# Performance work log

Hardware: AMD Instinct MI355X
Metric: run time of the kernel (lower is better)

Reference implementation:

```python
import jax, jax.numpy as jnp
import numpy as np
from jax.nn import relu, softplus, sigmoid

B, T, C, L = 256, 128, 16, 64
ENC, H, OBS_IN, NLAGS = 32, 64, 8, 24
SUBSTEPS = 2


def setup_inputs() -> dict:
    key = jax.random.key(0)
    ks = jax.random.split(key, 32)
    rn = lambda k, shp, s=0.1: jax.random.normal(k, shp, dtype=jnp.float32) * s
    return {
        "timestamps": jnp.linspace(0.0, 1.0, T, dtype=jnp.float32),
        "obs": rn(ks[0], (B, NLAGS, OBS_IN), 1.0),
        "coef_d": rn(ks[1], (B, T - 1, C)),
        "coef_c": rn(ks[2], (B, T - 1, C)),
        "coef_b": rn(ks[3], (B, T - 1, C)),
        "coef_a": rn(ks[4], (B, T - 1, C)),
        "gru_wih": rn(ks[5], (3 * H, OBS_IN)),
        "gru_whh": rn(ks[6], (3 * H, H)),
        "gru_bih": rn(ks[7], (3 * H,)),
        "gru_bhh": rn(ks[8], (3 * H,)),
        "gru_lin_w": rn(ks[9], (ENC, H)),
        "ie_w0": rn(ks[10], (128, ENC + C)),
        "ie_b0": rn(ks[11], (128,)),
        "ie_wh": rn(ks[12], (1, 128, 128)),
        "ie_bh": rn(ks[13], (1, 128)),
        "ie_wout": rn(ks[14], (L, 128)),
        "ie_bout": rn(ks[15], (L,)),
        "vf_w0": rn(ks[16], (128, L)),
        "vf_b0": rn(ks[17], (128,)),
        "vf_wh": rn(ks[18], (1, 128, 128)),
        "vf_bh": rn(ks[19], (1, 128)),
        "vf_wout": rn(ks[20], (L * C, 128)),
        "vf_bout": rn(ks[21], (L * C,)),
        "dec_w0": rn(ks[22], (L // 2, L)),
        "dec_b0": rn(ks[23], (L // 2,)),
        "dec_wh": rn(ks[24], (1, L // 2, L // 2)),
        "dec_bh": rn(ks[25], (1, L // 2)),
        "dec_wout": rn(ks[26], (8, L // 2)),
        "dec_bout": rn(ks[27], (8,)),
    }


def _mlp(x, w0, b0, wh, bh, wout, bout, act, fact):
    h = act(w0 @ x + b0)
    for i in range(wh.shape[0]):  # fixed small depth
        h = act(wh[i] @ h + bh[i])
    return fact(wout @ h + bout)


_ident = lambda v: v


def reference(timestamps, obs, coef_d, coef_c, coef_b, coef_a,
              gru_wih, gru_whh, gru_bih, gru_bhh, gru_lin_w,
              ie_w0, ie_b0, ie_wh, ie_bh, ie_wout, ie_bout,
              vf_w0, vf_b0, vf_wh, vf_bh, vf_wout, vf_bout,
              dec_w0, dec_b0, dec_wh, dec_bh, dec_wout, dec_bout):

    def single(obs_s, d_s, c_s, b_s, a_s):
        # --- GRU observation encoder ---
        def cell(h, x):
            gi = gru_wih @ x + gru_bih
            gh = gru_whh @ h + gru_bhh
            ir, iz, inn = jnp.split(gi, 3)
            hr, hz, hn = jnp.split(gh, 3)
            r = sigmoid(ir + hr)
            z = sigmoid(iz + hz)
            n = jnp.tanh(inn + r * hn)
            return (1.0 - z) * n + z * h, None
        hT, _ = jax.lax.scan(cell, jnp.zeros((H,), jnp.float32), obs_s)
        enc = gru_lin_w @ hT
        # control.evaluate(t0): cubic poly at frac=0 -> constant coeff a[0]
        x0 = a_s[0]
        y0 = _mlp(jnp.concatenate([enc, x0]), ie_w0, ie_b0, ie_wh, ie_bh, ie_wout, ie_bout, relu, _ident)

        def vf(y):
            return _mlp(y, vf_w0, vf_b0, vf_wh, vf_bh, vf_wout, vf_bout, softplus, jnp.tanh).reshape(L, C)

        js = jnp.arange(SUBSTEPS, dtype=jnp.float32)

        def interval(y, xs):
            t0, t1, di, ci, bi = xs
            hstep = (t1 - t0) / SUBSTEPS
            def f(frac, yy):
                dx = bi + 2.0 * ci * frac + 3.0 * di * frac * frac  # dX/dt on this interval
                return vf(yy) @ dx  # (L,)
            def sub(yy, j):  # one fixed Dopri5 step
                f0 = j * hstep
                k1 = f(f0, yy)
                k2 = f(f0 + hstep / 5, yy + hstep * (k1 / 5))
                k3 = f(f0 + 3 * hstep / 10, yy + hstep * (3 / 40 * k1 + 9 / 40 * k2))
                k4 = f(f0 + 4 * hstep / 5, yy + hstep * (44 / 45 * k1 - 56 / 15 * k2 + 32 / 9 * k3))
                k5 = f(f0 + 8 * hstep / 9, yy + hstep * (19372 / 6561 * k1 - 25360 / 2187 * k2 + 64448 / 6561 * k3 - 212 / 729 * k4))
                k6 = f(f0 + hstep, yy + hstep * (9017 / 3168 * k1 - 355 / 33 * k2 + 46732 / 5247 * k3 + 49 / 176 * k4 - 5103 / 18656 * k5))
                yn = yy + hstep * (35 / 384 * k1 + 500 / 1113 * k3 + 125 / 192 * k4 - 2187 / 6784 * k5 + 11 / 84 * k6)
                return yn, None
            y, _ = jax.lax.scan(jax.checkpoint(sub), y, js)
            return y, y

        xs = (timestamps[:-1], timestamps[1:], d_s, c_s, b_s)
        _, ys_rest = jax.lax.scan(interval, y0, xs)
        ys = jnp.concatenate([y0[None], ys_rest], axis=0)  # (T, L)
        dec = lambda yy: _mlp(yy, dec_w0, dec_b0, dec_wh, dec_bh, dec_wout, dec_bout, relu, _ident)
        return jax.vmap(dec)(ys)  # (T, state_size)

    return jax.vmap(single)(obs, coef_d, coef_c, coef_b, coef_a)  # (B, T, state_size)
```

## Files before the change

kernel.cpp:

```cpp
#include <hip/hip_runtime.h>
#include <hip/hip_fp16.h>

#define TPB 512

typedef _Float16 f16x8 __attribute__((ext_vector_type(8)));
typedef float f32x4 __attribute__((ext_vector_type(4)));

__device__ __forceinline__ float softplus_f(float x) {
    return fmaxf(x, 0.f) + __logf(1.f + __expf(-fabsf(x)));
}
__device__ __forceinline__ float tanh_f(float x) {
    float e = __expf(2.f * x);
    return 1.f - 2.f / (e + 1.f);
}
__device__ __forceinline__ float sigmoid_f(float x) {
    return 1.f / (1.f + __expf(-x));
}

__device__ __forceinline__ f32x4 mfma16(f16x8 a, f16x8 b, f32x4 c) {
    return __builtin_amdgcn_mfma_f32_16x16x32_f16(a, b, c, 0, 0, 0);
}

template <int CTRL>
__device__ __forceinline__ float dpp_add(float x) {
    int m = __builtin_amdgcn_update_dpp(0, __builtin_bit_cast(int, x), CTRL, 0xF, 0xF, true);
    return x + __builtin_bit_cast(float, m);
}

__global__ __launch_bounds__(TPB, 1) void ncde_kernel(
    const float* __restrict__ timestamps, const float* __restrict__ obs,
    const float* __restrict__ coef_d, const float* __restrict__ coef_c,
    const float* __restrict__ coef_b, const float* __restrict__ coef_a,
    const float* __restrict__ gru_wih, const float* __restrict__ gru_whh,
    const float* __restrict__ gru_bih, const float* __restrict__ gru_bhh,
    const float* __restrict__ gru_lin_w,
    const float* __restrict__ ie_w0, const float* __restrict__ ie_b0,
    const float* __restrict__ ie_wh, const float* __restrict__ ie_bh,
    const float* __restrict__ ie_wout, const float* __restrict__ ie_bout,
    const float* __restrict__ vf_w0, const float* __restrict__ vf_b0,
    const float* __restrict__ vf_wh, const float* __restrict__ vf_bh,
    const float* __restrict__ vf_wout, const float* __restrict__ vf_bout,
    const float* __restrict__ dec_w0, const float* __restrict__ dec_b0,
    const float* __restrict__ dec_wh, const float* __restrict__ dec_bh,
    const float* __restrict__ dec_wout, const float* __restrict__ dec_bout,
    float* __restrict__ out)
{
    const int b = blockIdx.x;
    const int tid = threadIdx.x;
    const int lane = tid & 63, wv = tid >> 6;
    const int m16 = lane & 15, g4 = lane >> 4;

    __shared__ __align__(16) float s_ysall[128][64];
    __shared__ __align__(16) float s_whh[192 * 65];
    __shared__ __align__(16) float s_wih[192 * 9];
    __shared__ __align__(16) float s_obs[24 * 8];
    __shared__ float s_gi[192];
    __shared__ float s_gh[192];
    __shared__ __align__(16) float s_y[64];
    __shared__ __align__(16) __half s_ysbh[64];
    __shared__ __align__(16) __half s_h1h[128];
    __shared__ __align__(16) __half s_h2h[128];
    __shared__ __align__(16) float s_V[1024];
    __shared__ __align__(16) float s_k[6][64];
    __shared__ float s_bi[16], s_ci[16], s_di[16];
    __shared__ __align__(16) float s_v48[48];
    __shared__ float s_m1[128], s_m2[128];

    for (int idx = tid; idx < 192 * 64; idx += TPB)
        s_whh[(idx >> 6) * 65 + (idx & 63)] = gru_whh[idx];
    for (int idx = tid; idx < 192 * 8; idx += TPB)
        s_wih[(idx >> 3) * 9 + (idx & 7)] = gru_wih[idx];
    if (tid < 24 * 8) s_obs[tid] = obs[(size_t)b * 192 + tid];
    const float bih_r = (tid < 192) ? gru_bih[tid] : 0.f;
    const float bhh_r = (tid < 192) ? gru_bhh[tid] : 0.f;
    if (tid < 64) s_y[tid] = 0.f;
    __syncthreads();

    for (int step = 0; step < 24; ++step) {
        if (tid < 192) {
            float gi = bih_r;
            const float* wr = &s_wih[tid * 9];
            const float* xr = &s_obs[step * 8];
#pragma unroll
            for (int j = 0; j < 8; ++j) gi = fmaf(wr[j], xr[j], gi);
            float g0 = bhh_r, g1 = 0.f, g2 = 0.f, g3 = 0.f;
            const float* hr = &s_whh[tid * 65];
#pragma unroll 4
            for (int j = 0; j < 64; j += 4) {
                g0 = fmaf(hr[j + 0], s_y[j + 0], g0);
                g1 = fmaf(hr[j + 1], s_y[j + 1], g1);
                g2 = fmaf(hr[j + 2], s_y[j + 2], g2);
                g3 = fmaf(hr[j + 3], s_y[j + 3], g3);
            }
            s_gi[tid] = gi;
            s_gh[tid] = (g0 + g1) + (g2 + g3);
        }
        __syncthreads();
        if (tid < 64) {
            float rg = sigmoid_f(s_gi[tid] + s_gh[tid]);
            float zg = sigmoid_f(s_gi[64 + tid] + s_gh[64 + tid]);
            float ng = tanh_f(s_gi[128 + tid] + rg * s_gh[128 + tid]);
            s_y[tid] = (1.f - zg) * ng + zg * s_y[tid];
        }
        __syncthreads();
    }

    if (tid < 32) {
        float e = 0.f;
        const float* wr = gru_lin_w + tid * 64;
        for (int j = 0; j < 64; ++j) e = fmaf(wr[j], s_y[j], e);
        s_v48[tid] = e;
    } else if (tid < 48) {
        s_v48[tid] = coef_a[(size_t)b * 127 * 16 + (tid - 32)];
    }
    __syncthreads();

    if (tid < 128) {
        float a = ie_b0[tid];
        const float* wr = ie_w0 + tid * 48;
        for (int j = 0; j < 48; ++j) a = fmaf(wr[j], s_v48[j], a);
        s_m1[tid] = fmaxf(a, 0.f);
    }
    __syncthreads();
    if (tid < 128) {
        float a = ie_bh[tid];
        const float* wr = ie_wh + tid * 128;
        for (int j = 0; j < 128; ++j) a = fmaf(wr[j], s_m1[j], a);
        s_m2[tid] = fmaxf(a, 0.f);
    }
    __syncthreads();
    if (tid < 64) {
        float a = ie_bout[tid];
        const float* wr = ie_wout + tid * 128;
        for (int j = 0; j < 128; ++j) a = fmaf(wr[j], s_m2[j], a);
        s_y[tid] = a;
        s_ysbh[tid] = __float2half_rn(a);
        s_ysall[0][tid] = a;
    }
    __syncthreads();

    f16x8 aw0[2], awh[4], awq[8][4];
    {
        const int row = wv * 16 + m16;
#pragma unroll
        for (int f = 0; f < 2; ++f) {
            f16x8 a;
#pragma unroll
            for (int j = 0; j < 8; ++j)
                a[j] = (_Float16)vf_w0[row * 64 + f * 32 + g4 * 8 + j];
            aw0[f] = a;
        }
#pragma unroll
        for (int f = 0; f < 4; ++f) {
            f16x8 a;
#pragma unroll
            for (int j = 0; j < 8; ++j)
                a[j] = (_Float16)vf_wh[row * 128 + f * 32 + g4 * 8 + j];
            awh[f] = a;
        }
#pragma unroll
        for (int i = 0; i < 8; ++i) {
            const int rq = (wv * 8 + i) * 16 + m16;
#pragma unroll
            for (int f = 0; f < 4; ++f) {
                f16x8 a;
#pragma unroll
                for (int j = 0; j < 8; ++j)
                    a[j] = (_Float16)vf_wout[(size_t)rq * 128 + f * 32 + g4 * 8 + j];
                awq[i][f] = a;
            }
        }
    }
    const float4 bw0 = *(const float4*)(vf_b0 + wv * 16 + g4 * 4);
    const float4 bwh = *(const float4*)(vf_bh + wv * 16 + g4 * 4);
    const float bo0 = vf_bout[2 * tid], bo1 = vf_bout[2 * tid + 1];
    const int l_idx = tid >> 3;
    const int c0 = 2 * (tid & 7);

    const size_t cofs = (size_t)b * 127 * 16;

#define KS(m) s_k[m][tid]
#define YS_PHASE(...)                                                          \
    do {                                                                       \
        if (tid < 64) {                                                        \
            float yv = s_y[tid];                                               \
            __VA_ARGS__;                                                       \
            s_ysbh[tid] = __float2half_rn(yv);                                 \
        }                                                                      \
        __syncthreads();                                                       \
    } while (0)

#define MFMA_STAGE(S, CC)                                                      \
    do {                                                                       \
        {                          \
            f16x8 b0 = *(const f16x8*)((const char*)s_ysbh + g4 * 16);         \
            f16x8 b1 = *(const f16x8*)((const char*)s_ysbh + 64 + g4 * 16);    \
            f32x4 acc = {0.f, 0.f, 0.f, 0.f};                                  \
            acc = mfma16(aw0[0], b0, acc);                                     \
            acc = mfma16(aw0[1], b1, acc);                                     \
            if (m16 == 0) {                                                    \
                __half q0 = __float2half_rn(softplus_f(acc[0] + bw0.x));       \
                __half q1 = __float2half_rn(softplus_f(acc[1] + bw0.y));       \
                __half q2 = __float2half_rn(softplus_f(acc[2] + bw0.z));       \
                __half q3 = __float2half_rn(softplus_f(acc[3] + bw0.w));       \
                uint2 pk;                                                      \
                pk.x = (unsigned)__half_as_ushort(q0) | ((unsigned)__half_as_ushort(q1) << 16); \
                pk.y = (unsigned)__half_as_ushort(q2) | ((unsigned)__half_as_ushort(q3) << 16); \
                *(uint2*)(&s_h1h[wv * 16 + g4 * 4]) = pk;                      \
            }                                                                  \
        }                                                                      \
        __syncthreads();                                                       \
        {                                                    \
            f32x4 acc = {0.f, 0.f, 0.f, 0.f};                                  \
            _Pragma("unroll")                                                  \
            for (int f = 0; f < 4; ++f) {                                      \
                f16x8 bf = *(const f16x8*)((const char*)s_h1h + f * 64 + g4 * 16); \
                acc = mfma16(awh[f], bf, acc);                                 \
            }                                                                  \
            if (m16 == 0) {                                                    \
                __half q0 = __float2half_rn(softplus_f(acc[0] + bwh.x));       \
                __half q1 = __float2half_rn(softplus_f(acc[1] + bwh.y));       \
                __half q2 = __float2half_rn(softplus_f(acc[2] + bwh.z));       \
                __half q3 = __float2half_rn(softplus_f(acc[3] + bwh.w));       \
                uint2 pk;                                                      \
                pk.x = (unsigned)__half_as_ushort(q0) | ((unsigned)__half_as_ushort(q1) << 16); \
                pk.y = (unsigned)__half_as_ushort(q2) | ((unsigned)__half_as_ushort(q3) << 16); \
                *(uint2*)(&s_h2h[wv * 16 + g4 * 4]) = pk;                      \
            }                                                                  \
        }                                                                      \
        __syncthreads();                                                       \
        {                     \
            f16x8 bf[4];                                                       \
            _Pragma("unroll")                                                  \
            for (int f = 0; f < 4; ++f)                                        \
                bf[f] = *(const f16x8*)((const char*)s_h2h + f * 64 + g4 * 16); \
            _Pragma("unroll")                                                  \
            for (int i = 0; i < 8; ++i) {                                      \
                f32x4 acc = {0.f, 0.f, 0.f, 0.f};                              \
                acc = mfma16(awq[i][0], bf[0], acc);                           \
                acc = mfma16(awq[i][1], bf[1], acc);                           \
                acc = mfma16(awq[i][2], bf[2], acc);                           \
                acc = mfma16(awq[i][3], bf[3], acc);                           \
                if (m16 == 0)                                                  \
                    *(f32x4*)(&s_V[(wv * 8 + i) * 16 + g4 * 4]) = acc;         \
            }                                                                  \
        }                                                                      \
        __syncthreads();                                                       \
        {              \
            float2 vp = *(const float2*)(&s_V[l_idx * 16 + c0]);               \
            float v0 = tanh_f(vp.x + bo0);                                     \
            float v1 = tanh_f(vp.y + bo1);                                     \
            float frac = fmaf((CC), hstep, f0);                                \
            float dx0 = fmaf(3.f * s_di[c0], frac * frac,                      \
                             fmaf(2.f * s_ci[c0], frac, s_bi[c0]));            \
            float dx1 = fmaf(3.f * s_di[c0 + 1], frac * frac,                  \
                             fmaf(2.f * s_ci[c0 + 1], frac, s_bi[c0 + 1]));    \
            float p = fmaf(v0, dx0, v1 * dx1);                                 \
            p = dpp_add<0xB1>(p);                                              \
            p = dpp_add<0x4E>(p);                                              \
            p = dpp_add<0x141>(p);                                             \
            if ((tid & 7) == 0) s_k[S][l_idx] = p;                             \
        }                                                                      \
        __syncthreads();                                                       \
    } while (0)

#pragma unroll 1
    for (int t = 0; t < 127; ++t) {
        if (tid < 16) s_bi[tid] = coef_b[cofs + t * 16 + tid];
        else if (tid < 32) s_ci[tid - 16] = coef_c[cofs + t * 16 + (tid - 16)];
        else if (tid < 48) s_di[tid - 32] = coef_d[cofs + t * 16 + (tid - 32)];
        const float t0 = timestamps[t], t1 = timestamps[t + 1];
        const float hstep = (t1 - t0) * 0.5f;

#pragma unroll 1
        for (int sub = 0; sub < 2; ++sub) {
            const float f0 = (float)sub * hstep;

            MFMA_STAGE(0, 0.f);
            YS_PHASE(yv = fmaf(hstep * 0.2f, KS(0), yv));
            MFMA_STAGE(1, 0.2f);
            YS_PHASE(yv = fmaf(hstep, fmaf(3.f / 40.f, KS(0), (9.f / 40.f) * KS(1)), yv));
            MFMA_STAGE(2, 0.3f);
            YS_PHASE(yv = fmaf(hstep, fmaf(44.f / 45.f, KS(0),
                          fmaf(-56.f / 15.f, KS(1), (32.f / 9.f) * KS(2))), yv));
            MFMA_STAGE(3, 0.8f);
            YS_PHASE(yv = fmaf(hstep, fmaf(19372.f / 6561.f, KS(0),
                          fmaf(-25360.f / 2187.f, KS(1),
                          fmaf(64448.f / 6561.f, KS(2), (-212.f / 729.f) * KS(3)))), yv));
            MFMA_STAGE(4, 8.f / 9.f);
            YS_PHASE(yv = fmaf(hstep, fmaf(9017.f / 3168.f, KS(0),
                          fmaf(-355.f / 33.f, KS(1),
                          fmaf(46732.f / 5247.f, KS(2),
                          fmaf(49.f / 176.f, KS(3), (-5103.f / 18656.f) * KS(4))))), yv));
            MFMA_STAGE(5, 1.f);

            if (tid < 64) {
                float yv = s_y[tid];
                yv = fmaf(hstep * (35.f / 384.f), s_k[0][tid], yv);
                yv = fmaf(hstep * (500.f / 1113.f), s_k[2][tid], yv);
                yv = fmaf(hstep * (125.f / 192.f), s_k[3][tid], yv);
                yv = fmaf(hstep * (-2187.f / 6784.f), s_k[4][tid], yv);
                yv = fmaf(hstep * (11.f / 84.f), s_k[5][tid], yv);
                s_y[tid] = yv;
                s_ysbh[tid] = __float2half_rn(yv);
                if (sub == 1) s_ysall[t + 1][tid] = yv;
            }
            __syncthreads();
        }
    }

    const int wid = tid >> 6, lane2 = tid & 63;
    for (int t = wid; t < 128; t += 8) {
        const float* yy = s_ysall[t];
        float h1d = 0.f;
        if (lane2 < 32) {
            float a = dec_b0[lane2];
            const float* wr = dec_w0 + lane2 * 64;
            for (int j = 0; j < 64; ++j) a = fmaf(wr[j], yy[j], a);
            h1d = fmaxf(a, 0.f);
        }
        float a2 = (lane2 < 32) ? dec_bh[lane2] : 0.f;
#pragma unroll 8
        for (int j = 0; j < 32; ++j) {
            float hj = __shfl(h1d, j);
            if (lane2 < 32) a2 = fmaf(dec_wh[lane2 * 32 + j], hj, a2);
        }
        float h2d = fmaxf(a2, 0.f);
        float o = (lane2 < 8) ? dec_bout[lane2] : 0.f;
#pragma unroll 8
        for (int j = 0; j < 32; ++j) {
            float hj = __shfl(h2d, j);
            if (lane2 < 8) o = fmaf(dec_wout[lane2 * 32 + j], hj, o);
        }
        if (lane2 < 8) out[(size_t)b * 1024 + t * 8 + lane2] = o;
    }
}

extern "C" void kernel_launch(void* const* d_in, const int* in_sizes, int n_in,
                              void* d_out, int out_size, void* d_ws, size_t ws_size,
                              hipStream_t stream) {
    const float* p[29];
    for (int i = 0; i < 29; ++i) p[i] = (const float*)d_in[i];
    ncde_kernel<<<256, TPB, 0, stream>>>(
        p[0], p[1], p[2], p[3], p[4], p[5], p[6], p[7], p[8], p[9], p[10],
        p[11], p[12], p[13], p[14], p[15], p[16], p[17], p[18], p[19], p[20],
        p[21], p[22], p[23], p[24], p[25], p[26], p[27], p[28],
        (float*)d_out);
}
```

Before: 2.855 ms.

## Replace output-layer MFMA with per-thread fp16 dot2 and fuse stage updates

The 1024x128 vector-field output layer is now computed per thread: each thread holds its two weight rows packed as fp16 pairs in registers and uses fdot2 against the hidden vector in shared memory. This removes the s_V staging buffer and one barrier per stage. The RK stage-state update is folded into the lane that writes each k value, which removes the separate YS phase and its barrier. The cost is 128 extra VGPRs of weights per thread, which raises register pressure and may spill, plus more scalar ALU work in place of matrix instructions.

```diff
diff --git a/kernel.cpp b/kernel.cpp
--- a/kernel.cpp
+++ b/kernel.cpp
@@ -3,8 +3,25 @@
 
 #define TPB 512
 
+typedef _Float16 h2v __attribute__((ext_vector_type(2)));
 typedef _Float16 f16x8 __attribute__((ext_vector_type(8)));
 typedef float f32x4 __attribute__((ext_vector_type(4)));
+
+__device__ __forceinline__ float dot2f(unsigned int a, unsigned int b, float c) {
+#if __has_builtin(__builtin_amdgcn_fdot2)
+    return __builtin_amdgcn_fdot2(__builtin_bit_cast(h2v, a), __builtin_bit_cast(h2v, b), c, false);
+#else
+    float2 af = __half22float2(__builtin_bit_cast(__half2, a));
+    float2 bf = __half22float2(__builtin_bit_cast(__half2, b));
+    return fmaf(af.y, bf.y, fmaf(af.x, bf.x, c));
+#endif
+}
+
+__device__ __forceinline__ unsigned int pack2(float a, float b) {
+    unsigned int lo = (unsigned int)__half_as_ushort(__float2half_rn(a));
+    unsigned int hi = (unsigned int)__half_as_ushort(__float2half_rn(b));
+    return lo | (hi << 16);
+}
 
 __device__ __forceinline__ float softplus_f(float x) {
     return fmaxf(x, 0.f) + __logf(1.f + __expf(-fabsf(x)));
@@ -60,7 +77,6 @@
     __shared__ __align__(16) __half s_ysbh[64];
     __shared__ __align__(16) __half s_h1h[128];
     __shared__ __align__(16) __half s_h2h[128];
-    __shared__ __align__(16) float s_V[1024];
     __shared__ __align__(16) float s_k[6][64];
     __shared__ float s_bi[16], s_ci[16], s_di[16];
     __shared__ __align__(16) float s_v48[48];
@@ -139,7 +155,16 @@
     }
     __syncthreads();
 
-    f16x8 aw0[2], awh[4], awq[8][4];
+    unsigned int wq0[64], wq1[64];
+    {
+        const float* r0 = vf_wout + (size_t)(2 * tid) * 128;
+#pragma unroll
+        for (int j = 0; j < 64; ++j) wq0[j] = pack2(r0[2 * j], r0[2 * j + 1]);
+        const float* r1 = r0 + 128;
+#pragma unroll
+        for (int j = 0; j < 64; ++j) wq1[j] = pack2(r1[2 * j], r1[2 * j + 1]);
+    }
+    f16x8 aw0[2], awh[4];
     {
         const int row = wv * 16 + m16;
 #pragma unroll
@@ -157,18 +182,6 @@
             for (int j = 0; j < 8; ++j)
                 a[j] = (_Float16)vf_wh[row * 128 + f * 32 + g4 * 8 + j];
             awh[f] = a;
-        }
-#pragma unroll
-        for (int i = 0; i < 8; ++i) {
-            const int rq = (wv * 8 + i) * 16 + m16;
-#pragma unroll
-            for (int f = 0; f < 4; ++f) {
-                f16x8 a;
-#pragma unroll
-                for (int j = 0; j < 8; ++j)
-                    a[j] = (_Float16)vf_wout[(size_t)rq * 128 + f * 32 + g4 * 8 + j];
-                awq[i][f] = a;
-            }
         }
     }
     const float4 bw0 = *(const float4*)(vf_b0 + wv * 16 + g4 * 4);
@@ -179,33 +192,18 @@
 
     const size_t cofs = (size_t)b * 127 * 16;
 
-#define KS(m) s_k[m][tid]
-#define YS_PHASE(...)                                                          \
+#define VF_STAGE(S, CC, ...)                                                   \
     do {                                                                       \
-        if (tid < 64) {                                                        \
-            float yv = s_y[tid];                                               \
-            __VA_ARGS__;                                                       \
-            s_ysbh[tid] = __float2half_rn(yv);                                 \
-        }                                                                      \
-        __syncthreads();                                                       \
-    } while (0)
-
-#define MFMA_STAGE(S, CC)                                                      \
-    do {                                                                       \
-        {                          \
+        {    \
             f16x8 b0 = *(const f16x8*)((const char*)s_ysbh + g4 * 16);         \
             f16x8 b1 = *(const f16x8*)((const char*)s_ysbh + 64 + g4 * 16);    \
             f32x4 acc = {0.f, 0.f, 0.f, 0.f};                                  \
             acc = mfma16(aw0[0], b0, acc);                                     \
             acc = mfma16(aw0[1], b1, acc);                                     \
             if (m16 == 0) {                                                    \
-                __half q0 = __float2half_rn(softplus_f(acc[0] + bw0.x));       \
-                __half q1 = __float2half_rn(softplus_f(acc[1] + bw0.y));       \
-                __half q2 = __float2half_rn(softplus_f(acc[2] + bw0.z));       \
-                __half q3 = __float2half_rn(softplus_f(acc[3] + bw0.w));       \
                 uint2 pk;                                                      \
-                pk.x = (unsigned)__half_as_ushort(q0) | ((unsigned)__half_as_ushort(q1) << 16); \
-                pk.y = (unsigned)__half_as_ushort(q2) | ((unsigned)__half_as_ushort(q3) << 16); \
+                pk.x = pack2(softplus_f(acc[0] + bw0.x), softplus_f(acc[1] + bw0.y)); \
+                pk.y = pack2(softplus_f(acc[2] + bw0.z), softplus_f(acc[3] + bw0.w)); \
                 *(uint2*)(&s_h1h[wv * 16 + g4 * 4]) = pk;                      \
             }                                                                  \
         }                                                                      \
@@ -218,38 +216,29 @@
                 acc = mfma16(awh[f], bf, acc);                                 \
             }                                                                  \
             if (m16 == 0) {                                                    \
-                __half q0 = __float2half_rn(softplus_f(acc[0] + bwh.x));       \
-                __half q1 = __float2half_rn(softplus_f(acc[1] + bwh.y));       \
-                __half q2 = __float2half_rn(softplus_f(acc[2] + bwh.z));       \
-                __half q3 = __float2half_rn(softplus_f(acc[3] + bwh.w));       \
                 uint2 pk;                                                      \
-                pk.x = (unsigned)__half_as_ushort(q0) | ((unsigned)__half_as_ushort(q1) << 16); \
-                pk.y = (unsigned)__half_as_ushort(q2) | ((unsigned)__half_as_ushort(q3) << 16); \
+                pk.x = pack2(softplus_f(acc[0] + bwh.x), softplus_f(acc[1] + bwh.y)); \
+                pk.y = pack2(softplus_f(acc[2] + bwh.z), softplus_f(acc[3] + bwh.w)); \
                 *(uint2*)(&s_h2h[wv * 16 + g4 * 4]) = pk;                      \
             }                                                                  \
         }                                                                      \
         __syncthreads();                                                       \
-        {                     \
-            f16x8 bf[4];                                                       \
+        {                       \
+            float a0 = 0.f, a1 = 0.f, b0a = 0.f, b1a = 0.f;                    \
             _Pragma("unroll")                                                  \
-            for (int f = 0; f < 4; ++f)                                        \
-                bf[f] = *(const f16x8*)((const char*)s_h2h + f * 64 + g4 * 16); \
-            _Pragma("unroll")                                                  \
-            for (int i = 0; i < 8; ++i) {                                      \
-                f32x4 acc = {0.f, 0.f, 0.f, 0.f};                              \
-                acc = mfma16(awq[i][0], bf[0], acc);                           \
-                acc = mfma16(awq[i][1], bf[1], acc);                           \
-                acc = mfma16(awq[i][2], bf[2], acc);                           \
-                acc = mfma16(awq[i][3], bf[3], acc);                           \
-                if (m16 == 0)                                                  \
-                    *(f32x4*)(&s_V[(wv * 8 + i) * 16 + g4 * 4]) = acc;         \
-            }                                                                  \
-        }                                                                      \
-        __syncthreads();                                                       \
-        {              \
-            float2 vp = *(const float2*)(&s_V[l_idx * 16 + c0]);               \
-            float v0 = tanh_f(vp.x + bo0);                                     \
-            float v1 = tanh_f(vp.y + bo1);                                     \
+            for (int k4 = 0; k4 < 16; ++k4) {                                  \
+                uint4 hv = *reinterpret_cast<const uint4*>(&s_h2h[8 * k4]);    \
+                a0 = dot2f(wq0[4 * k4 + 0], hv.x, a0);                         \
+                b0a = dot2f(wq1[4 * k4 + 0], hv.x, b0a);                       \
+                a1 = dot2f(wq0[4 * k4 + 1], hv.y, a1);                         \
+                b1a = dot2f(wq1[4 * k4 + 1], hv.y, b1a);                       \
+                a0 = dot2f(wq0[4 * k4 + 2], hv.z, a0);                         \
+                b0a = dot2f(wq1[4 * k4 + 2], hv.z, b0a);                       \
+                a1 = dot2f(wq0[4 * k4 + 3], hv.w, a1);                         \
+                b1a = dot2f(wq1[4 * k4 + 3], hv.w, b1a);                       \
+            }                                                                  \
+            float v0 = tanh_f(a0 + a1 + bo0);                                  \
+            float v1 = tanh_f(b0a + b1a + bo1);                                \
             float frac = fmaf((CC), hstep, f0);                                \
             float dx0 = fmaf(3.f * s_di[c0], frac * frac,                      \
                              fmaf(2.f * s_ci[c0], frac, s_bi[c0]));            \
@@ -258,8 +247,11 @@
             float p = fmaf(v0, dx0, v1 * dx1);                                 \
             p = dpp_add<0xB1>(p);                                              \
             p = dpp_add<0x4E>(p);                                              \
-            p = dpp_add<0x141>(p);                                             \
-            if ((tid & 7) == 0) s_k[S][l_idx] = p;                             \
+            p = dpp_add<0x141>(p);          \
+            if ((tid & 7) == 0) {                                              \
+                s_k[(S)][l_idx] = p;                                           \
+                __VA_ARGS__   \
+            }                                                                  \
         }                                                                      \
         __syncthreads();                                                       \
     } while (0)
@@ -276,23 +268,36 @@
         for (int sub = 0; sub < 2; ++sub) {
             const float f0 = (float)sub * hstep;
 
-            MFMA_STAGE(0, 0.f);
-            YS_PHASE(yv = fmaf(hstep * 0.2f, KS(0), yv));
-            MFMA_STAGE(1, 0.2f);
-            YS_PHASE(yv = fmaf(hstep, fmaf(3.f / 40.f, KS(0), (9.f / 40.f) * KS(1)), yv));
-            MFMA_STAGE(2, 0.3f);
-            YS_PHASE(yv = fmaf(hstep, fmaf(44.f / 45.f, KS(0),
-                          fmaf(-56.f / 15.f, KS(1), (32.f / 9.f) * KS(2))), yv));
-            MFMA_STAGE(3, 0.8f);
-            YS_PHASE(yv = fmaf(hstep, fmaf(19372.f / 6561.f, KS(0),
-                          fmaf(-25360.f / 2187.f, KS(1),
-                          fmaf(64448.f / 6561.f, KS(2), (-212.f / 729.f) * KS(3)))), yv));
-            MFMA_STAGE(4, 8.f / 9.f);
-            YS_PHASE(yv = fmaf(hstep, fmaf(9017.f / 3168.f, KS(0),
-                          fmaf(-355.f / 33.f, KS(1),
-                          fmaf(46732.f / 5247.f, KS(2),
-                          fmaf(49.f / 176.f, KS(3), (-5103.f / 18656.f) * KS(4))))), yv));
-            MFMA_STAGE(5, 1.f);
+            VF_STAGE(0, 0.f, {
+                float ys = fmaf(hstep * 0.2f, p, s_y[l_idx]);
+                s_ysbh[l_idx] = __float2half_rn(ys);
+            });
+            VF_STAGE(1, 0.2f, {
+                float ys = fmaf(hstep,
+                    fmaf(3.f / 40.f, s_k[0][l_idx], (9.f / 40.f) * p), s_y[l_idx]);
+                s_ysbh[l_idx] = __float2half_rn(ys);
+            });
+            VF_STAGE(2, 0.3f, {
+                float ys = fmaf(hstep, fmaf(44.f / 45.f, s_k[0][l_idx],
+                    fmaf(-56.f / 15.f, s_k[1][l_idx], (32.f / 9.f) * p)), s_y[l_idx]);
+                s_ysbh[l_idx] = __float2half_rn(ys);
+            });
+            VF_STAGE(3, 0.8f, {
+                float ys = fmaf(hstep, fmaf(19372.f / 6561.f, s_k[0][l_idx],
+                    fmaf(-25360.f / 2187.f, s_k[1][l_idx],
+                    fmaf(64448.f / 6561.f, s_k[2][l_idx], (-212.f / 729.f) * p))),
+                    s_y[l_idx]);
+                s_ysbh[l_idx] = __float2half_rn(ys);
+            });
+            VF_STAGE(4, 8.f / 9.f, {
+                float ys = fmaf(hstep, fmaf(9017.f / 3168.f, s_k[0][l_idx],
+                    fmaf(-355.f / 33.f, s_k[1][l_idx],
+                    fmaf(46732.f / 5247.f, s_k[2][l_idx],
+                    fmaf(49.f / 176.f, s_k[3][l_idx], (-5103.f / 18656.f) * p)))),
+                    s_y[l_idx]);
+                s_ysbh[l_idx] = __float2half_rn(ys);
+            });
+            VF_STAGE(5, 1.f, {});
 
             if (tid < 64) {
                 float yv = s_y[tid];
```

Measured after the change: 2.765 ms. -3.1%, faster.
